# Kernel optimization log

Hardware: AMD Instinct MI355X
Metric: run time of the kernel (lower is better)

Reference implementation:

```python
import jax, jax.numpy as jnp
import numpy as np

B, C, H, W = 8, 256, 32, 32
N_HEAD = 4
EPS = 1e-5


def setup_inputs() -> dict:
    key = jax.random.key(0)
    ks = jax.random.split(key, 8)
    return {
        "input": jax.random.normal(ks[0], (B, C, H, W), dtype=jnp.float32),
        "bn_gamma": jnp.ones((C,), dtype=jnp.float32),
        "bn_beta": jnp.zeros((C,), dtype=jnp.float32),
        "bn_mean": jax.random.normal(ks[1], (C,), dtype=jnp.float32) * 0.1,
        "bn_var": jax.random.uniform(ks[2], (C,), dtype=jnp.float32, minval=0.5, maxval=1.5),
        "dw_w": jax.random.normal(ks[3], (C,), dtype=jnp.float32) * (1.0 / np.sqrt(C)),
        "pw_w": jax.random.normal(ks[4], (3 * C, C), dtype=jnp.float32) * (1.0 / np.sqrt(C)),
        "out_w": jax.random.normal(ks[5], (C, C), dtype=jnp.float32) * (1.0 / np.sqrt(C)),
        "out_b": jnp.zeros((C,), dtype=jnp.float32),
    }


def reference(input, bn_gamma, bn_beta, bn_mean, bn_var, dw_w, pw_w, out_w, out_b):
    b, c, h, w = input.shape
    n_head = N_HEAD
    head_dim = c // n_head

    # BatchNorm2d (eval mode: running stats), fused with depthwise 1x1 conv
    # (groups=C, kernel 1x1 -> per-channel scalar multiply).
    scale = (bn_gamma * jax.lax.rsqrt(bn_var + EPS) * dw_w)[None, :, None, None]
    shift = (bn_beta * dw_w)[None, :, None, None]
    mean = bn_mean[None, :, None, None]
    x = (input - mean) * scale + shift  # [B,C,H,W]

    # Pointwise 1x1 conv -> QKV: [B, 3C, H, W]
    qkv = jnp.einsum('oc,bchw->bohw', pw_w, x)
    qkv = qkv.reshape(b, n_head, head_dim * 3, h, w)
    q, k, v = jnp.split(qkv, 3, axis=2)  # each [B,n,d,H,W]

    # Full spatial attention logits: [B, n, H, W, H, W]
    attn = jnp.einsum('bnchw,bncyx->bnhwyx', q, k) * (1.0 / np.sqrt(head_dim))
    # Faithful to original: softmax over LAST axis (key x/width) ONLY.
    attn = jax.nn.softmax(attn, axis=-1)

    out = jnp.einsum('bnhwyx,bncyx->bnchw', attn, v).reshape(b, c, h, w)
    out = jnp.einsum('oc,bchw->bohw', out_w, out) + out_b[None, :, None, None]
    return out + input
```

## Files before the change

kernel.cpp:

```cpp
#include <hip/hip_runtime.h>

#define NB 8
#define NC 256
#define NS 1024
#define NHEAD 4
#define HD 64
#define OC 768

typedef float f32x4 __attribute__((ext_vector_type(4)));
typedef __bf16 bf16x8 __attribute__((ext_vector_type(8)));
typedef unsigned short u16;
typedef unsigned int u32;
typedef u16 u16x8 __attribute__((ext_vector_type(8)));
typedef u32 u32x2 __attribute__((ext_vector_type(2)));
typedef int i32x4 __attribute__((ext_vector_type(4)));

__device__ __forceinline__ u16 f2b(float f) {
    union { float f; unsigned u; } v; v.f = f;
    return (u16)((v.u + 0x7FFFu + ((v.u >> 16) & 1u)) >> 16);
}
__device__ __forceinline__ u32 pack2(float lo, float hi) {
    return (u32)f2b(lo) | ((u32)f2b(hi) << 16);
}

__device__ __forceinline__ f32x4 MFMA(u16x8 a, u16x8 b, f32x4 c) {
    return __builtin_amdgcn_mfma_f32_16x16x32_bf16(
        __builtin_bit_cast(bf16x8, a), __builtin_bit_cast(bf16x8, b), c, 0, 0, 0);
}

__global__ void xform(const float* __restrict__ in,
                      const float* __restrict__ gma, const float* __restrict__ bta,
                      const float* __restrict__ mu,  const float* __restrict__ var,
                      const float* __restrict__ dw,  u16* __restrict__ xt) {
    __shared__ float tile[32][33];
    __shared__ float ssc[32], ssh[32];
    int b = blockIdx.z, c0 = blockIdx.y * 32, s0 = blockIdx.x * 32;
    int tx = threadIdx.x & 31, ty = threadIdx.x >> 5;
    if (threadIdx.x < 32) {
        int c = c0 + threadIdx.x;
        float sc = gma[c] * rsqrtf(var[c] + 1e-5f) * dw[c];
        ssc[threadIdx.x] = sc;
        ssh[threadIdx.x] = bta[c] * dw[c] - mu[c] * sc;
    }
    __syncthreads();
#pragma unroll
    for (int r = 0; r < 4; r++) {
        int c = ty + r * 8;
        tile[c][tx] = in[((size_t)b * NC + c0 + c) * NS + s0 + tx] * ssc[c] + ssh[c];
    }
    __syncthreads();
#pragma unroll
    for (int r = 0; r < 4; r++) {
        int s = ty + r * 8;
        xt[((size_t)b * NS + s0 + s) * NC + c0 + tx] = f2b(tile[tx][s]);
    }
}

#define BKP 56
__global__ __launch_bounds__(256) void qkv_gemm(const float* __restrict__ pw, const u16* __restrict__ xt,
                                                u16* __restrict__ qb, u16* __restrict__ kb,
                                                u16* __restrict__ vb) {
    __shared__ __attribute__((aligned(16))) u16 Ws[64][BKP];
    __shared__ __attribute__((aligned(16))) u16 Xs[128][BKP];
    int b = blockIdx.z;
    int m0 = blockIdx.y * 64, n0 = blockIdx.x * 128;
    int tid = threadIdx.x, lane = tid & 63, w = tid >> 6, lg = lane >> 4, li = lane & 15;
    int rowA = tid >> 2, colA = (tid & 3) * 8;
    int rowB = tid >> 1, colB = (tid & 1) * 16;
    const float* pA = pw + (size_t)(m0 + rowA) * NC + colA;
    const u16*   pB = xt + ((size_t)b * NS + n0 + rowB) * NC + colB;
    f32x4 acc[4][2] = {};
#pragma unroll
    for (int k0 = 0; k0 < NC; k0 += 32) {
        __syncthreads();
        f32x4 a0 = *(const f32x4*)(pA + k0);
        f32x4 a1 = *(const f32x4*)(pA + k0 + 4);
        i32x4 tb0 = *(const i32x4*)(pB + k0);
        i32x4 tb1 = *(const i32x4*)(pB + k0 + 8);
        i32x4 wa;
        wa[0] = pack2(a0[0], a0[1]); wa[1] = pack2(a0[2], a0[3]);
        wa[2] = pack2(a1[0], a1[1]); wa[3] = pack2(a1[2], a1[3]);
        *(i32x4*)&Ws[rowA][colA] = wa;
        *(i32x4*)&Xs[rowB][colB]     = tb0;
        *(i32x4*)&Xs[rowB][colB + 8] = tb1;
        __syncthreads();
        u16x8 af[4], bfr[2];
#pragma unroll
        for (int mf = 0; mf < 4; mf++) af[mf] = *(const u16x8*)&Ws[mf * 16 + li][lg * 8];
#pragma unroll
        for (int nf = 0; nf < 2; nf++) bfr[nf] = *(const u16x8*)&Xs[w * 32 + nf * 16 + li][lg * 8];
#pragma unroll
        for (int mf = 0; mf < 4; mf++)
#pragma unroll
            for (int nf = 0; nf < 2; nf++)
                acc[mf][nf] = MFMA(af[mf], bfr[nf], acc[mf][nf]);
    }
#pragma unroll
    for (int mf = 0; mf < 4; mf++) {
#pragma unroll
        for (int j = 0; j < 4; j++) {
            int o = m0 + mf * 16 + lg * 4 + j;
            int n = o / 192, r = o - n * 192;
            size_t bn = (size_t)b * NHEAD + n;
#pragma unroll
            for (int nf = 0; nf < 2; nf++) {
                int s = n0 + w * 32 + nf * 16 + li;
                u16 v = f2b(acc[mf][nf][j]);
                if (r < 64)       qb[(bn * NS + s) * HD + r] = v;
                else if (r < 128) kb[(bn * NS + s) * HD + (r - 64)] = v;
                else              vb[(bn * HD + (r - 128)) * NS + s] = v;
            }
        }
    }
}

__global__ __launch_bounds__(256) void attn_k(const u16* __restrict__ qbuf, const u16* __restrict__ kbuf,
                                              const u16* __restrict__ vbuf, u16* __restrict__ ao0,
                                              u16* __restrict__ ao1) {
    __shared__ __attribute__((aligned(16))) u16 Qs[64][72], Ks[64][72], Vs[64][72];
    __shared__ __attribute__((aligned(16))) u16 Ps[4][16][72];
    int b = blockIdx.z, n = blockIdx.y;
    int s0 = (blockIdx.x >> 1) * 64;
    int th = blockIdx.x & 1;
    u16* aoh = th ? ao1 : ao0;
    size_t bn = (size_t)b * NHEAD + n;
    const u16* qg = qbuf + (bn * NS + s0) * HD;
    const u16* kg = kbuf + (bn * NS + th * 512) * HD;
    const u16* vg = vbuf + bn * HD * NS + th * 512;
    int tid = threadIdx.x, lane = tid & 63, w = tid >> 6, lg = lane >> 4, li = lane & 15;
    int srow = tid >> 2, sc8 = (tid & 3) * 16;
    *(i32x4*)&Qs[srow][sc8]     = *(const i32x4*)(qg + srow * HD + sc8);
    *(i32x4*)&Qs[srow][sc8 + 8] = *(const i32x4*)(qg + srow * HD + sc8 + 8);
    i32x4 rk0 = *(const i32x4*)(kg + srow * HD + sc8);
    i32x4 rk1 = *(const i32x4*)(kg + srow * HD + sc8 + 8);
    i32x4 rv0 = *(const i32x4*)(vg + srow * NS + sc8);
    i32x4 rv1 = *(const i32x4*)(vg + srow * NS + sc8 + 8);
    __syncthreads();
    u16x8 bq0 = *(const u16x8*)&Qs[w * 16 + li][lg * 8];
    u16x8 bq1 = *(const u16x8*)&Qs[w * 16 + li][32 + lg * 8];
    f32x4 oacc[4] = {};
    const float sc = 0.125f * 1.4426950408889634f;
    for (int t0 = 0; t0 < 512; t0 += 64) {
        *(i32x4*)&Ks[srow][sc8]     = rk0;
        *(i32x4*)&Ks[srow][sc8 + 8] = rk1;
        *(i32x4*)&Vs[srow][sc8]     = rv0;
        *(i32x4*)&Vs[srow][sc8 + 8] = rv1;
        __syncthreads();
        if (t0 + 64 < 512) {
            rk0 = *(const i32x4*)(kg + (t0 + 64 + srow) * HD + sc8);
            rk1 = *(const i32x4*)(kg + (t0 + 64 + srow) * HD + sc8 + 8);
            rv0 = *(const i32x4*)(vg + srow * NS + t0 + 64 + sc8);
            rv1 = *(const i32x4*)(vg + srow * NS + t0 + 64 + sc8 + 8);
        }
        f32x4 sacc[4];
#pragma unroll
        for (int tf = 0; tf < 4; tf++) {
            u16x8 ak0 = *(const u16x8*)&Ks[tf * 16 + li][lg * 8];
            u16x8 ak1 = *(const u16x8*)&Ks[tf * 16 + li][32 + lg * 8];
            f32x4 z = {0.f, 0.f, 0.f, 0.f};
            z = MFMA(ak0, bq0, z);
            sacc[tf] = MFMA(ak1, bq1, z);
        }
        u32x2 pp[4];
#pragma unroll
        for (int g = 0; g < 2; g++) {
            float mx = sacc[2 * g][0];
#pragma unroll
            for (int j = 1; j < 4; j++) mx = fmaxf(mx, sacc[2 * g][j]);
#pragma unroll
            for (int j = 0; j < 4; j++) mx = fmaxf(mx, sacc[2 * g + 1][j]);
            mx = fmaxf(mx, __shfl_xor(mx, 16));
            mx = fmaxf(mx, __shfl_xor(mx, 32));
            float p[8];
            float sum = 0.f;
#pragma unroll
            for (int j = 0; j < 4; j++) { p[j] = exp2f((sacc[2 * g][j] - mx) * sc); sum += p[j]; }
#pragma unroll
            for (int j = 0; j < 4; j++) { p[4 + j] = exp2f((sacc[2 * g + 1][j] - mx) * sc); sum += p[4 + j]; }
            sum += __shfl_xor(sum, 16);
            sum += __shfl_xor(sum, 32);
            float inv = 1.0f / sum;
#pragma unroll
            for (int tt = 0; tt < 2; tt++) {
                u32 lo = pack2(p[tt * 4 + 0] * inv, p[tt * 4 + 1] * inv);
                u32 hi = pack2(p[tt * 4 + 2] * inv, p[tt * 4 + 3] * inv);
                u32x2 pk; pk[0] = lo; pk[1] = hi;
                pp[2 * g + tt] = pk;
            }
        }
#pragma unroll
        for (int tf = 0; tf < 4; tf++)
            *(u32x2*)&Ps[w][li][tf * 16 + lg * 4] = pp[tf];
        u16x8 pa0 = *(const u16x8*)&Ps[w][li][lg * 8];
        u16x8 pa1 = *(const u16x8*)&Ps[w][li][32 + lg * 8];
#pragma unroll
        for (int nf = 0; nf < 4; nf++) {
            u16x8 bv0 = *(const u16x8*)&Vs[nf * 16 + li][lg * 8];
            u16x8 bv1 = *(const u16x8*)&Vs[nf * 16 + li][32 + lg * 8];
            oacc[nf] = MFMA(pa0, bv0, oacc[nf]);
            oacc[nf] = MFMA(pa1, bv1, oacc[nf]);
        }
        __syncthreads();
    }
#pragma unroll
    for (int nf = 0; nf < 4; nf++)
#pragma unroll
        for (int j = 0; j < 4; j++) {
            int s = s0 + w * 16 + lg * 4 + j;
            int c = n * HD + nf * 16 + li;
            aoh[((size_t)b * NS + s) * NC + c] = f2b(oacc[nf][j]);
        }
}

__global__ __launch_bounds__(256) void out_gemm(const float* __restrict__ ow, const u16* __restrict__ ao0,
                                                const u16* __restrict__ ao1,
                                                const float* __restrict__ outb, const float* __restrict__ in,
                                                float* __restrict__ out) {
    __shared__ __attribute__((aligned(16))) u16 Ws[64][BKP];
    __shared__ __attribute__((aligned(16))) u16 Xs[128][BKP];
    int b = blockIdx.z;
    int m0 = blockIdx.y * 64, n0 = blockIdx.x * 128;
    int tid = threadIdx.x, lane = tid & 63, w = tid >> 6, lg = lane >> 4, li = lane & 15;
    int rowA = tid >> 2, colA = (tid & 3) * 8;
    int rowB = tid >> 1, colB = (tid & 1) * 16;
    const float* pA = ow + (size_t)(m0 + rowA) * NC + colA;
    size_t boff = ((size_t)b * NS + n0 + rowB) * NC + colB;
    f32x4 acc[4][2] = {};
#pragma unroll
    for (int k0 = 0; k0 < 2 * NC; k0 += 32) {
        const u16* pB = (k0 < NC ? ao0 : ao1) + boff + (k0 & (NC - 1));
        int ka = k0 & (NC - 1);
        __syncthreads();
        f32x4 a0 = *(const f32x4*)(pA + ka);
        f32x4 a1 = *(const f32x4*)(pA + ka + 4);
        i32x4 tb0 = *(const i32x4*)(pB);
        i32x4 tb1 = *(const i32x4*)(pB + 8);
        i32x4 wa;
        wa[0] = pack2(a0[0], a0[1]); wa[1] = pack2(a0[2], a0[3]);
        wa[2] = pack2(a1[0], a1[1]); wa[3] = pack2(a1[2], a1[3]);
        *(i32x4*)&Ws[rowA][colA] = wa;
        *(i32x4*)&Xs[rowB][colB]     = tb0;
        *(i32x4*)&Xs[rowB][colB + 8] = tb1;
        __syncthreads();
        u16x8 af[4], bfr[2];
#pragma unroll
        for (int mf = 0; mf < 4; mf++) af[mf] = *(const u16x8*)&Ws[mf * 16 + li][lg * 8];
#pragma unroll
        for (int nf = 0; nf < 2; nf++) bfr[nf] = *(const u16x8*)&Xs[w * 32 + nf * 16 + li][lg * 8];
#pragma unroll
        for (int mf = 0; mf < 4; mf++)
#pragma unroll
            for (int nf = 0; nf < 2; nf++)
                acc[mf][nf] = MFMA(af[mf], bfr[nf], acc[mf][nf]);
    }
#pragma unroll
    for (int mf = 0; mf < 4; mf++)
#pragma unroll
        for (int j = 0; j < 4; j++) {
            int o = m0 + mf * 16 + lg * 4 + j;
            float bias = outb[o];
#pragma unroll
            for (int nf = 0; nf < 2; nf++) {
                int s = n0 + w * 32 + nf * 16 + li;
                size_t idx = ((size_t)b * NC + o) * NS + s;
                out[idx] = acc[mf][nf][j] + bias + in[idx];
            }
        }
}

extern "C" void kernel_launch(void* const* d_in, const int* in_sizes, int n_in,
                              void* d_out, int out_size, void* d_ws, size_t ws_size,
                              hipStream_t stream) {
    const float* input = (const float*)d_in[0];
    const float* gma = (const float*)d_in[1];
    const float* bta = (const float*)d_in[2];
    const float* mu  = (const float*)d_in[3];
    const float* var = (const float*)d_in[4];
    const float* dw  = (const float*)d_in[5];
    const float* pw  = (const float*)d_in[6];
    const float* ow  = (const float*)d_in[7];
    const float* ob  = (const float*)d_in[8];
    float* out = (float*)d_out;
    char* ws = (char*)d_ws;

    const size_t SZ_BIG = (size_t)NB * NS * NC * 2;
    u16* xt  = (u16*)(ws);
    u16* qb  = (u16*)(ws + SZ_BIG);
    u16* kb  = (u16*)(ws + 2 * SZ_BIG);
    u16* vb  = (u16*)(ws + 3 * SZ_BIG);
    u16* ao1 = (u16*)(ws + 4 * SZ_BIG);
    u16* ao0 = xt;

    xform<<<dim3(32, 8, 8), 256, 0, stream>>>(input, gma, bta, mu, var, dw, xt);
    qkv_gemm<<<dim3(8, 12, 8), 256, 0, stream>>>(pw, xt, qb, kb, vb);
    attn_k<<<dim3(32, 4, 8), 256, 0, stream>>>(qb, kb, vb, ao0, ao1);
    out_gemm<<<dim3(8, 4, 8), 256, 0, stream>>>(ow, ao0, ao1, ob, input, out);
}
```

Measured before the change: 73.08 us.

## Split attention key tile across warps and double GEMM K-step

The attention kernel now has each warp handle 32 queries against half of the 64-key tile, so K and V fragments are reused across two query fragments. Partial outputs from the two key halves are reduced through shared memory at the end. MFMA sections are wrapped in s_setprio. Both GEMM kernels move from a K-step of 32 to 64 with wider padded LDS tiles, halving the barrier count per output tile, at the cost of more LDS use and registers.

New measurement: 69.92 us. -4.3%, faster.

```diff
diff --git a/kernel.cpp b/kernel.cpp
--- a/kernel.cpp
+++ b/kernel.cpp
@@ -56,44 +56,60 @@
     }
 }
 
-#define BKP 56
 __global__ __launch_bounds__(256) void qkv_gemm(const float* __restrict__ pw, const u16* __restrict__ xt,
                                                 u16* __restrict__ qb, u16* __restrict__ kb,
                                                 u16* __restrict__ vb) {
-    __shared__ __attribute__((aligned(16))) u16 Ws[64][BKP];
-    __shared__ __attribute__((aligned(16))) u16 Xs[128][BKP];
+    __shared__ __attribute__((aligned(16))) u16 Ws[64][72];
+    __shared__ __attribute__((aligned(16))) u16 Xs[128][72];
     int b = blockIdx.z;
     int m0 = blockIdx.y * 64, n0 = blockIdx.x * 128;
     int tid = threadIdx.x, lane = tid & 63, w = tid >> 6, lg = lane >> 4, li = lane & 15;
-    int rowA = tid >> 2, colA = (tid & 3) * 8;
-    int rowB = tid >> 1, colB = (tid & 1) * 16;
+    int rowA = tid >> 2, colA = (tid & 3) * 16;
+    int rowB = tid >> 1, colB = (tid & 1) * 32;
     const float* pA = pw + (size_t)(m0 + rowA) * NC + colA;
     const u16*   pB = xt + ((size_t)b * NS + n0 + rowB) * NC + colB;
     f32x4 acc[4][2] = {};
 #pragma unroll
-    for (int k0 = 0; k0 < NC; k0 += 32) {
+    for (int k0 = 0; k0 < NC; k0 += 64) {
         __syncthreads();
         f32x4 a0 = *(const f32x4*)(pA + k0);
         f32x4 a1 = *(const f32x4*)(pA + k0 + 4);
+        f32x4 a2 = *(const f32x4*)(pA + k0 + 8);
+        f32x4 a3 = *(const f32x4*)(pA + k0 + 12);
         i32x4 tb0 = *(const i32x4*)(pB + k0);
         i32x4 tb1 = *(const i32x4*)(pB + k0 + 8);
-        i32x4 wa;
-        wa[0] = pack2(a0[0], a0[1]); wa[1] = pack2(a0[2], a0[3]);
-        wa[2] = pack2(a1[0], a1[1]); wa[3] = pack2(a1[2], a1[3]);
-        *(i32x4*)&Ws[rowA][colA] = wa;
-        *(i32x4*)&Xs[rowB][colB]     = tb0;
-        *(i32x4*)&Xs[rowB][colB + 8] = tb1;
-        __syncthreads();
-        u16x8 af[4], bfr[2];
-#pragma unroll
-        for (int mf = 0; mf < 4; mf++) af[mf] = *(const u16x8*)&Ws[mf * 16 + li][lg * 8];
-#pragma unroll
-        for (int nf = 0; nf < 2; nf++) bfr[nf] = *(const u16x8*)&Xs[w * 32 + nf * 16 + li][lg * 8];
+        i32x4 tb2 = *(const i32x4*)(pB + k0 + 16);
+        i32x4 tb3 = *(const i32x4*)(pB + k0 + 24);
+        i32x4 wa0, wa1;
+        wa0[0] = pack2(a0[0], a0[1]); wa0[1] = pack2(a0[2], a0[3]);
+        wa0[2] = pack2(a1[0], a1[1]); wa0[3] = pack2(a1[2], a1[3]);
+        wa1[0] = pack2(a2[0], a2[1]); wa1[1] = pack2(a2[2], a2[3]);
+        wa1[2] = pack2(a3[0], a3[1]); wa1[3] = pack2(a3[2], a3[3]);
+        *(i32x4*)&Ws[rowA][colA]     = wa0;
+        *(i32x4*)&Ws[rowA][colA + 8] = wa1;
+        *(i32x4*)&Xs[rowB][colB]      = tb0;
+        *(i32x4*)&Xs[rowB][colB + 8]  = tb1;
+        *(i32x4*)&Xs[rowB][colB + 16] = tb2;
+        *(i32x4*)&Xs[rowB][colB + 24] = tb3;
+        __syncthreads();
+        u16x8 af[4][2], bfr[2][2];
 #pragma unroll
         for (int mf = 0; mf < 4; mf++)
 #pragma unroll
-            for (int nf = 0; nf < 2; nf++)
-                acc[mf][nf] = MFMA(af[mf], bfr[nf], acc[mf][nf]);
+            for (int kc = 0; kc < 2; kc++)
+                af[mf][kc] = *(const u16x8*)&Ws[mf * 16 + li][kc * 32 + lg * 8];
+#pragma unroll
+        for (int nf = 0; nf < 2; nf++)
+#pragma unroll
+            for (int kc = 0; kc < 2; kc++)
+                bfr[nf][kc] = *(const u16x8*)&Xs[w * 32 + nf * 16 + li][kc * 32 + lg * 8];
+#pragma unroll
+        for (int kc = 0; kc < 2; kc++)
+#pragma unroll
+            for (int mf = 0; mf < 4; mf++)
+#pragma unroll
+                for (int nf = 0; nf < 2; nf++)
+                    acc[mf][nf] = MFMA(af[mf][kc], bfr[nf][kc], acc[mf][nf]);
     }
 #pragma unroll
     for (int mf = 0; mf < 4; mf++) {
@@ -114,11 +130,20 @@
     }
 }
 
+#define SMEM_Q 0
+#define SMEM_K 9216
+#define SMEM_V 18432
+#define SMEM_P 27648
+#define SMEM_BYTES 37888
 __global__ __launch_bounds__(256) void attn_k(const u16* __restrict__ qbuf, const u16* __restrict__ kbuf,
                                               const u16* __restrict__ vbuf, u16* __restrict__ ao0,
                                               u16* __restrict__ ao1) {
-    __shared__ __attribute__((aligned(16))) u16 Qs[64][72], Ks[64][72], Vs[64][72];
-    __shared__ __attribute__((aligned(16))) u16 Ps[4][16][72];
+    __shared__ __attribute__((aligned(16))) char smem[SMEM_BYTES];
+    u16 (*Qs)[72] = (u16(*)[72])(smem + SMEM_Q);
+    u16 (*Ks)[72] = (u16(*)[72])(smem + SMEM_K);
+    u16 (*Vs)[72] = (u16(*)[72])(smem + SMEM_V);
+    u16 (*Ps)[32][40] = (u16(*)[32][40])(smem + SMEM_P);
+    float (*red)[68] = (float(*)[68])smem;
     int b = blockIdx.z, n = blockIdx.y;
     int s0 = (blockIdx.x >> 1) * 64;
     int th = blockIdx.x & 1;
@@ -128,6 +153,7 @@
     const u16* kg = kbuf + (bn * NS + th * 512) * HD;
     const u16* vg = vbuf + bn * HD * NS + th * 512;
     int tid = threadIdx.x, lane = tid & 63, w = tid >> 6, lg = lane >> 4, li = lane & 15;
+    int tq = w & 1, tt = w >> 1;
     int srow = tid >> 2, sc8 = (tid & 3) * 16;
     *(i32x4*)&Qs[srow][sc8]     = *(const i32x4*)(qg + srow * HD + sc8);
     *(i32x4*)&Qs[srow][sc8 + 8] = *(const i32x4*)(qg + srow * HD + sc8 + 8);
@@ -136,11 +162,16 @@
     i32x4 rv0 = *(const i32x4*)(vg + srow * NS + sc8);
     i32x4 rv1 = *(const i32x4*)(vg + srow * NS + sc8 + 8);
     __syncthreads();
-    u16x8 bq0 = *(const u16x8*)&Qs[w * 16 + li][lg * 8];
-    u16x8 bq1 = *(const u16x8*)&Qs[w * 16 + li][32 + lg * 8];
-    f32x4 oacc[4] = {};
+    u16x8 bq[2][2];
+#pragma unroll
+    for (int qf = 0; qf < 2; qf++)
+#pragma unroll
+        for (int kc = 0; kc < 2; kc++)
+            bq[qf][kc] = *(const u16x8*)&Qs[tq * 32 + qf * 16 + li][kc * 32 + lg * 8];
+    f32x4 oacc[2][4] = {};
     const float sc = 0.125f * 1.4426950408889634f;
     for (int t0 = 0; t0 < 512; t0 += 64) {
+        __syncthreads();
         *(i32x4*)&Ks[srow][sc8]     = rk0;
         *(i32x4*)&Ks[srow][sc8 + 8] = rk1;
         *(i32x4*)&Vs[srow][sc8]     = rv0;
@@ -152,106 +183,154 @@
             rv0 = *(const i32x4*)(vg + srow * NS + t0 + 64 + sc8);
             rv1 = *(const i32x4*)(vg + srow * NS + t0 + 64 + sc8 + 8);
         }
-        f32x4 sacc[4];
-#pragma unroll
-        for (int tf = 0; tf < 4; tf++) {
-            u16x8 ak0 = *(const u16x8*)&Ks[tf * 16 + li][lg * 8];
-            u16x8 ak1 = *(const u16x8*)&Ks[tf * 16 + li][32 + lg * 8];
-            f32x4 z = {0.f, 0.f, 0.f, 0.f};
-            z = MFMA(ak0, bq0, z);
-            sacc[tf] = MFMA(ak1, bq1, z);
-        }
-        u32x2 pp[4];
-#pragma unroll
-        for (int g = 0; g < 2; g++) {
-            float mx = sacc[2 * g][0];
-#pragma unroll
-            for (int j = 1; j < 4; j++) mx = fmaxf(mx, sacc[2 * g][j]);
-#pragma unroll
-            for (int j = 0; j < 4; j++) mx = fmaxf(mx, sacc[2 * g + 1][j]);
+        u16x8 ak[2][2];
+#pragma unroll
+        for (int tf = 0; tf < 2; tf++)
+#pragma unroll
+            for (int kc = 0; kc < 2; kc++)
+                ak[tf][kc] = *(const u16x8*)&Ks[tt * 32 + tf * 16 + li][kc * 32 + lg * 8];
+        f32x4 sacc[2][2];
+        __builtin_amdgcn_s_setprio(1);
+#pragma unroll
+        for (int tf = 0; tf < 2; tf++)
+#pragma unroll
+            for (int qf = 0; qf < 2; qf++) {
+                f32x4 z = {0.f, 0.f, 0.f, 0.f};
+                z = MFMA(ak[tf][0], bq[qf][0], z);
+                sacc[tf][qf] = MFMA(ak[tf][1], bq[qf][1], z);
+            }
+        __builtin_amdgcn_s_setprio(0);
+        u32x2 pp[2][2];
+#pragma unroll
+        for (int qf = 0; qf < 2; qf++) {
+            float mx = sacc[0][qf][0];
+#pragma unroll
+            for (int j = 1; j < 4; j++) mx = fmaxf(mx, sacc[0][qf][j]);
+#pragma unroll
+            for (int j = 0; j < 4; j++) mx = fmaxf(mx, sacc[1][qf][j]);
             mx = fmaxf(mx, __shfl_xor(mx, 16));
             mx = fmaxf(mx, __shfl_xor(mx, 32));
             float p[8];
             float sum = 0.f;
 #pragma unroll
-            for (int j = 0; j < 4; j++) { p[j] = exp2f((sacc[2 * g][j] - mx) * sc); sum += p[j]; }
-#pragma unroll
-            for (int j = 0; j < 4; j++) { p[4 + j] = exp2f((sacc[2 * g + 1][j] - mx) * sc); sum += p[4 + j]; }
+            for (int j = 0; j < 4; j++) { p[j] = exp2f((sacc[0][qf][j] - mx) * sc); sum += p[j]; }
+#pragma unroll
+            for (int j = 0; j < 4; j++) { p[4 + j] = exp2f((sacc[1][qf][j] - mx) * sc); sum += p[4 + j]; }
             sum += __shfl_xor(sum, 16);
             sum += __shfl_xor(sum, 32);
             float inv = 1.0f / sum;
 #pragma unroll
-            for (int tt = 0; tt < 2; tt++) {
-                u32 lo = pack2(p[tt * 4 + 0] * inv, p[tt * 4 + 1] * inv);
-                u32 hi = pack2(p[tt * 4 + 2] * inv, p[tt * 4 + 3] * inv);
-                u32x2 pk; pk[0] = lo; pk[1] = hi;
-                pp[2 * g + tt] = pk;
+            for (int tf = 0; tf < 2; tf++) {
+                u32x2 pk;
+                pk[0] = pack2(p[tf * 4 + 0] * inv, p[tf * 4 + 1] * inv);
+                pk[1] = pack2(p[tf * 4 + 2] * inv, p[tf * 4 + 3] * inv);
+                pp[qf][tf] = pk;
             }
         }
 #pragma unroll
-        for (int tf = 0; tf < 4; tf++)
-            *(u32x2*)&Ps[w][li][tf * 16 + lg * 4] = pp[tf];
-        u16x8 pa0 = *(const u16x8*)&Ps[w][li][lg * 8];
-        u16x8 pa1 = *(const u16x8*)&Ps[w][li][32 + lg * 8];
-#pragma unroll
-        for (int nf = 0; nf < 4; nf++) {
-            u16x8 bv0 = *(const u16x8*)&Vs[nf * 16 + li][lg * 8];
-            u16x8 bv1 = *(const u16x8*)&Vs[nf * 16 + li][32 + lg * 8];
-            oacc[nf] = MFMA(pa0, bv0, oacc[nf]);
-            oacc[nf] = MFMA(pa1, bv1, oacc[nf]);
-        }
-        __syncthreads();
-    }
-#pragma unroll
-    for (int nf = 0; nf < 4; nf++)
-#pragma unroll
-        for (int j = 0; j < 4; j++) {
-            int s = s0 + w * 16 + lg * 4 + j;
-            int c = n * HD + nf * 16 + li;
-            aoh[((size_t)b * NS + s) * NC + c] = f2b(oacc[nf][j]);
-        }
+        for (int qf = 0; qf < 2; qf++)
+#pragma unroll
+            for (int tf = 0; tf < 2; tf++)
+                *(u32x2*)&Ps[w][qf * 16 + li][tf * 16 + lg * 4] = pp[qf][tf];
+        u16x8 pa[2];
+#pragma unroll
+        for (int qf = 0; qf < 2; qf++)
+            pa[qf] = *(const u16x8*)&Ps[w][qf * 16 + li][lg * 8];
+        u16x8 bv[4];
+#pragma unroll
+        for (int nf = 0; nf < 4; nf++)
+            bv[nf] = *(const u16x8*)&Vs[nf * 16 + li][tt * 32 + lg * 8];
+        __builtin_amdgcn_s_setprio(1);
+#pragma unroll
+        for (int qf = 0; qf < 2; qf++)
+#pragma unroll
+            for (int nf = 0; nf < 4; nf++)
+                oacc[qf][nf] = MFMA(pa[qf], bv[nf], oacc[qf][nf]);
+        __builtin_amdgcn_s_setprio(0);
+    }
+    __syncthreads();
+    if (tt == 1) {
+#pragma unroll
+        for (int qf = 0; qf < 2; qf++)
+#pragma unroll
+            for (int nf = 0; nf < 4; nf++)
+#pragma unroll
+                for (int j = 0; j < 4; j++)
+                    red[tq * 32 + qf * 16 + lg * 4 + j][nf * 16 + li] = oacc[qf][nf][j];
+    }
+    __syncthreads();
+    if (tt == 0) {
+#pragma unroll
+        for (int qf = 0; qf < 2; qf++)
+#pragma unroll
+            for (int nf = 0; nf < 4; nf++)
+#pragma unroll
+                for (int j = 0; j < 4; j++) {
+                    int s = s0 + tq * 32 + qf * 16 + lg * 4 + j;
+                    int c = n * HD + nf * 16 + li;
+                    float v = oacc[qf][nf][j] + red[tq * 32 + qf * 16 + lg * 4 + j][nf * 16 + li];
+                    aoh[((size_t)b * NS + s) * NC + c] = f2b(v);
+                }
+    }
 }
 
 __global__ __launch_bounds__(256) void out_gemm(const float* __restrict__ ow, const u16* __restrict__ ao0,
                                                 const u16* __restrict__ ao1,
                                                 const float* __restrict__ outb, const float* __restrict__ in,
                                                 float* __restrict__ out) {
-    __shared__ __attribute__((aligned(16))) u16 Ws[64][BKP];
-    __shared__ __attribute__((aligned(16))) u16 Xs[128][BKP];
+    __shared__ __attribute__((aligned(16))) u16 Ws[64][72];
+    __shared__ __attribute__((aligned(16))) u16 Xs[128][72];
     int b = blockIdx.z;
     int m0 = blockIdx.y * 64, n0 = blockIdx.x * 128;
     int tid = threadIdx.x, lane = tid & 63, w = tid >> 6, lg = lane >> 4, li = lane & 15;
-    int rowA = tid >> 2, colA = (tid & 3) * 8;
-    int rowB = tid >> 1, colB = (tid & 1) * 16;
+    int rowA = tid >> 2, colA = (tid & 3) * 16;
+    int rowB = tid >> 1, colB = (tid & 1) * 32;
     const float* pA = ow + (size_t)(m0 + rowA) * NC + colA;
     size_t boff = ((size_t)b * NS + n0 + rowB) * NC + colB;
     f32x4 acc[4][2] = {};
 #pragma unroll
-    for (int k0 = 0; k0 < 2 * NC; k0 += 32) {
+    for (int k0 = 0; k0 < 2 * NC; k0 += 64) {
         const u16* pB = (k0 < NC ? ao0 : ao1) + boff + (k0 & (NC - 1));
         int ka = k0 & (NC - 1);
         __syncthreads();
         f32x4 a0 = *(const f32x4*)(pA + ka);
         f32x4 a1 = *(const f32x4*)(pA + ka + 4);
+        f32x4 a2 = *(const f32x4*)(pA + ka + 8);
+        f32x4 a3 = *(const f32x4*)(pA + ka + 12);
         i32x4 tb0 = *(const i32x4*)(pB);
         i32x4 tb1 = *(const i32x4*)(pB + 8);
-        i32x4 wa;
-        wa[0] = pack2(a0[0], a0[1]); wa[1] = pack2(a0[2], a0[3]);
-        wa[2] = pack2(a1[0], a1[1]); wa[3] = pack2(a1[2], a1[3]);
-        *(i32x4*)&Ws[rowA][colA] = wa;
-        *(i32x4*)&Xs[rowB][colB]     = tb0;
-        *(i32x4*)&Xs[rowB][colB + 8] = tb1;
-        __syncthreads();
-        u16x8 af[4], bfr[2];
-#pragma unroll
-        for (int mf = 0; mf < 4; mf++) af[mf] = *(const u16x8*)&Ws[mf * 16 + li][lg * 8];
-#pragma unroll
-        for (int nf = 0; nf < 2; nf++) bfr[nf] = *(const u16x8*)&Xs[w * 32 + nf * 16 + li][lg * 8];
+        i32x4 tb2 = *(const i32x4*)(pB + 16);
+        i32x4 tb3 = *(const i32x4*)(pB + 24);
+        i32x4 wa0, wa1;
+        wa0[0] = pack2(a0[0], a0[1]); wa0[1] = pack2(a0[2], a0[3]);
+        wa0[2] = pack2(a1[0], a1[1]); wa0[3] = pack2(a1[2], a1[3]);
+        wa1[0] = pack2(a2[0], a2[1]); wa1[1] = pack2(a2[2], a2[3]);
+        wa1[2] = pack2(a3[0], a3[1]); wa1[3] = pack2(a3[2], a3[3]);
+        *(i32x4*)&Ws[rowA][colA]     = wa0;
+        *(i32x4*)&Ws[rowA][colA + 8] = wa1;
+        *(i32x4*)&Xs[rowB][colB]      = tb0;
+        *(i32x4*)&Xs[rowB][colB + 8]  = tb1;
+        *(i32x4*)&Xs[rowB][colB + 16] = tb2;
+        *(i32x4*)&Xs[rowB][colB + 24] = tb3;
+        __syncthreads();
+        u16x8 af[4][2], bfr[2][2];
 #pragma unroll
         for (int mf = 0; mf < 4; mf++)
 #pragma unroll
-            for (int nf = 0; nf < 2; nf++)
-                acc[mf][nf] = MFMA(af[mf], bfr[nf], acc[mf][nf]);
+            for (int kc = 0; kc < 2; kc++)
+                af[mf][kc] = *(const u16x8*)&Ws[mf * 16 + li][kc * 32 + lg * 8];
+#pragma unroll
+        for (int nf = 0; nf < 2; nf++)
+#pragma unroll
+            for (int kc = 0; kc < 2; kc++)
+                bfr[nf][kc] = *(const u16x8*)&Xs[w * 32 + nf * 16 + li][kc * 32 + lg * 8];
+#pragma unroll
+        for (int kc = 0; kc < 2; kc++)
+#pragma unroll
+            for (int mf = 0; mf < 4; mf++)
+#pragma unroll
+                for (int nf = 0; nf < 2; nf++)
+                    acc[mf][nf] = MFMA(af[mf][kc], bfr[nf][kc], acc[mf][nf]);
     }
 #pragma unroll
     for (int mf = 0; mf < 4; mf++)
```
